# Kernel tuning notes

Measured on AMD Instinct MI355X. Metric: run time of the kernel, lower is better.

## Reference

```python
import jax, jax.numpy as jnp
import numpy as np

B, S, D, H, T = 64, 512, 1024, 1024, 9


def setup_inputs() -> dict:
    key = jax.random.key(0)
    ks = jax.random.split(key, 8)
    return {
        "input_": jax.random.normal(ks[0], (B, S, D), dtype=jnp.float32),
        "labels": jax.random.randint(ks[1], (B, S), 0, T),
        "attention_mask": jnp.ones((B, S), dtype=jnp.int32),
        # linear_1: input_dim -> hidden_dim (stored [in, out])
        "W1": (jax.random.normal(ks[2], (D, H), dtype=jnp.float32) * 0.02),
        "b1": jnp.zeros((H,), dtype=jnp.float32),
        # linear_2: hidden_dim -> tag_dim
        "W2": (jax.random.normal(ks[3], (H, T), dtype=jnp.float32) * 0.02),
        "b2": jnp.zeros((T,), dtype=jnp.float32),
        # torchcrf params: uniform(-0.1, 0.1)
        "start_trans": jax.random.uniform(ks[4], (T,), minval=-0.1, maxval=0.1),
        "end_trans": jax.random.uniform(ks[5], (T,), minval=-0.1, maxval=0.1),
        "trans": jax.random.uniform(ks[6], (T, T), minval=-0.1, maxval=0.1),
    }


def _crf_mean_llh(logits, tags, mask, start, end, trans):
    """torchcrf.CRF log-likelihood, reduction='mean'. logits [B,S,T]."""
    nb = logits.shape[0]
    em = jnp.transpose(logits, (1, 0, 2))          # [S,B,T] time-major
    tg = tags.T                                    # [S,B]
    m = mask.T.astype(logits.dtype)                # [S,B]
    bidx = jnp.arange(nb)

    # --- numerator: score of the gold path ---
    score0 = start[tg[0]] + em[0, bidx, tg[0]]

    def num_step(carry, x):
        score, last = carry
        em_t, tag_t, m_t = x
        score = score + (trans[last, tag_t] + em_t[bidx, tag_t]) * m_t
        last = jnp.where(m_t > 0, tag_t, last)
        return (score, last), None

    (score, last), _ = jax.lax.scan(num_step, (score0, tg[0]), (em[1:], tg[1:], m[1:]))
    score = score + end[last]

    # --- denominator: log-partition via logsumexp forward recurrence ---
    alpha0 = start[None, :] + em[0]                # [B,T]

    def part_step(alpha, x):
        em_t, m_t = x
        # [B, prev T, next T] semiring (log-sum-exp) matrix product
        nxt = jax.nn.logsumexp(alpha[:, :, None] + trans[None, :, :] + em_t[:, None, :], axis=1)
        alpha = jnp.where(m_t[:, None] > 0, nxt, alpha)
        return alpha, None

    alpha, _ = jax.lax.scan(part_step, alpha0, (em[1:], m[1:]))
    log_z = jax.nn.logsumexp(alpha + end[None, :], axis=1)

    return jnp.mean(score - log_z)


def reference(input_, labels, attention_mask, W1, b1, W2, b2, start_trans, end_trans, trans):
    # dropout layers are identity in eval mode
    h = input_ @ W1 + b1                           # [B,S,H]
    logits = h @ W2 + b2                           # [B,S,T]
    llh = _crf_mean_llh(logits, labels, attention_mask, start_trans, end_trans, trans)
    loss = -llh                                    # forward returns (-1*crf_llh, logits)
    return (loss, logits)
```

## Files before the change

### kernel.cpp

```cpp
#include <hip/hip_runtime.h>

#define BD 64
#define SD 512
#define DD 1024
#define HD 1024
#define TD 9
#define NSEG 16
#define SEGL 32
#define NEGI -1e30f

__device__ __forceinline__ float lse9(const float v[9]) {
    float m0 = fmaxf(v[0], v[1]);
    float m1 = fmaxf(v[2], v[3]);
    float m2 = fmaxf(v[4], v[5]);
    float m3 = fmaxf(v[6], v[7]);
    float mx = fmaxf(fmaxf(m0, m1), fmaxf(fmaxf(m2, m3), v[8]));
    float s = __expf(v[0] - mx) + __expf(v[1] - mx) + __expf(v[2] - mx)
            + __expf(v[3] - mx) + __expf(v[4] - mx) + __expf(v[5] - mx)
            + __expf(v[6] - mx) + __expf(v[7] - mx) + __expf(v[8] - mx);
    return mx + __logf(s);
}

__global__ __launch_bounds__(256) void k_w12(const float* __restrict__ W1,
                                             const float* __restrict__ b1,
                                             const float* __restrict__ W2,
                                             const float* __restrict__ b2,
                                             float* __restrict__ W12t,
                                             float* __restrict__ b12,
                                             float* __restrict__ out) {
    __shared__ float wred[4][TD];
    const int tid = threadIdx.x;
    const int wave = tid >> 6, lane = tid & 63;
    const int d = blockIdx.x;

    if (d == 0 && tid == 0) out[0] = 0.f;

    const float* row = (d < DD) ? (W1 + (size_t)d * HD) : b1;
    float4 x = ((const float4*)row)[tid];

    float w[36];
    const float4* wp = (const float4*)(W2 + (size_t)tid * 36);
#pragma unroll
    for (int u = 0; u < 9; u++) ((float4*)w)[u] = wp[u];

    float acc[TD];
#pragma unroll
    for (int t = 0; t < TD; t++)
        acc[t] = x.x * w[t] + x.y * w[9 + t] + x.z * w[18 + t] + x.w * w[27 + t];

#pragma unroll
    for (int t = 0; t < TD; t++) {
        float v = acc[t];
#pragma unroll
        for (int m = 1; m < 64; m <<= 1) v += __shfl_xor(v, m);
        acc[t] = v;
    }
    if (lane == 0) {
#pragma unroll
        for (int t = 0; t < TD; t++) wred[wave][t] = acc[t];
    }
    __syncthreads();
    if (tid < TD) {
        float s = wred[0][tid] + wred[1][tid] + wred[2][tid] + wred[3][tid];
        if (d < DD) W12t[tid * DD + d] = s;
        else        b12[tid] = s + b2[tid];
    }
}

__global__ __launch_bounds__(256) void k_gemm_seg(const float* __restrict__ X,
                                                  const float* __restrict__ W12t,
                                                  const float* __restrict__ b12,
                                                  const int* __restrict__ maskp,
                                                  const float* __restrict__ transp,
                                                  float* __restrict__ logits,
                                                  float* __restrict__ segP) {
    __shared__ float smem[TD * DD];
    __shared__ float em[SEGL * TD];
    __shared__ int   mk[SEGL];
    __shared__ float tr[81];
    __shared__ float bb[TD];

    const int blk = blockIdx.x;
    const int b = blk >> 4, s = blk & 15;
    const int tid = threadIdx.x;
    const int wave = tid >> 6, lane = tid & 63;
    const int g = lane >> 4, l16 = lane & 15;
    const int grp = wave * 4 + g;
    const int t0 = s * SEGL;

    for (int i = tid; i < TD * DD / 4; i += 256)
        ((float4*)smem)[i] = ((const float4*)W12t)[i];
    if (tid < TD) bb[tid] = b12[tid];
    if (tid < 81) tr[tid] = transp[tid];
    if (tid < SEGL) {
        int t = t0 + 1 + tid;
        mk[tid] = (t < SD) ? maskp[b * SD + t] : 0;
    }
    __syncthreads();

    const int rowa = t0 + 1 + grp * 2;
    const int rowb_real = rowa + 1;
    const int rowb = (rowb_real < SD) ? rowb_real : (SD - 1);

    const float4* xr0 = (const float4*)(X + ((size_t)b * SD + rowa) * DD);
    const float4* xr1 = (const float4*)(X + ((size_t)b * SD + rowb) * DD);

    float acc0[TD], acc1[TD];
#pragma unroll
    for (int t = 0; t < TD; t++) { acc0[t] = 0.f; acc1[t] = 0.f; }

#pragma unroll 4
    for (int k = 0; k < 16; k++) {
        int d4 = l16 + k * 16;
        float4 x0 = xr0[d4];
        float4 x1 = xr1[d4];
#pragma unroll
        for (int t = 0; t < TD; t++) {
            const float4 w = *(const float4*)&smem[t * DD + d4 * 4];
            acc0[t] += x0.x * w.x + x0.y * w.y + x0.z * w.z + x0.w * w.w;
            acc1[t] += x1.x * w.x + x1.y * w.y + x1.z * w.z + x1.w * w.w;
        }
    }

#pragma unroll
    for (int t = 0; t < TD; t++) {
        float v0 = acc0[t], v1 = acc1[t];
        v0 += __shfl_xor(v0, 1); v1 += __shfl_xor(v1, 1);
        v0 += __shfl_xor(v0, 2); v1 += __shfl_xor(v1, 2);
        v0 += __shfl_xor(v0, 4); v1 += __shfl_xor(v1, 4);
        v0 += __shfl_xor(v0, 8); v1 += __shfl_xor(v1, 8);
        acc0[t] = v0; acc1[t] = v1;
    }

    if (l16 < TD) {
        float v0 = acc0[l16] + bb[l16];
        float v1 = acc1[l16] + bb[l16];
        float* o = logits + ((size_t)b * SD + rowa) * TD;
        o[l16] = v0;
        em[(grp * 2) * TD + l16] = v0;
        if (rowb_real < SD) {
            o[TD + l16] = v1;
            em[(grp * 2 + 1) * TD + l16] = v1;
        }
    }

    if (s == 0 && grp == 0) {
        const float4* xr = (const float4*)(X + (size_t)b * SD * DD);
        float accz[TD];
#pragma unroll
        for (int t = 0; t < TD; t++) accz[t] = 0.f;
#pragma unroll 4
        for (int k = 0; k < 16; k++) {
            int d4 = l16 + k * 16;
            float4 xz = xr[d4];
#pragma unroll
            for (int t = 0; t < TD; t++) {
                const float4 w = *(const float4*)&smem[t * DD + d4 * 4];
                accz[t] += xz.x * w.x + xz.y * w.y + xz.z * w.z + xz.w * w.w;
            }
        }
#pragma unroll
        for (int t = 0; t < TD; t++) {
            float v = accz[t];
            v += __shfl_xor(v, 1);
            v += __shfl_xor(v, 2);
            v += __shfl_xor(v, 4);
            v += __shfl_xor(v, 8);
            accz[t] = v;
        }
        if (l16 < TD) logits[(size_t)b * SD * TD + l16] = accz[l16] + bb[l16];
    }
    __syncthreads();

    float* bufA = smem;
    float* bufB = smem + 16 * 81;

    for (int e = tid; e < 16 * 81; e += 256) {
        int p = e / 81, r = e - p * 81;
        int i = r / 9, j = r - i * 9;
        int la = 2 * p, lb = 2 * p + 1;
        int mA = mk[la], mB = mk[lb];
        float o;
        if (mA && mB) {
            float v[9];
#pragma unroll
            for (int k = 0; k < 9; k++)
                v[k] = tr[i * 9 + k] + em[la * 9 + k] + tr[k * 9 + j];
            o = lse9(v) + em[lb * 9 + j];
        } else if (mA) {
            o = tr[r] + em[la * 9 + j];
        } else if (mB) {
            o = tr[r] + em[lb * 9 + j];
        } else {
            o = (i == j) ? 0.f : NEGI;
        }
        bufA[e] = o;
    }
    __syncthreads();

#define COMBINE(SRC, DST, NP)                                        \
    for (int e = tid; e < (NP) * 81; e += 256) {                     \
        int p = e / 81, r = e - p * 81;                              \
        int i = r / 9, j = r - i * 9;                                \
        const float* Am = (SRC) + (2 * p) * 81;                      \
        const float* Bm = Am + 81;                                   \
        float v[9];                                                  \
        _Pragma("unroll")                                            \
        for (int k = 0; k < 9; k++) v[k] = Am[i * 9 + k] + Bm[k * 9 + j]; \
        (DST)[e] = lse9(v);                                          \
    }                                                                \
    __syncthreads();

    COMBINE(bufA, bufB, 8)
    COMBINE(bufB, bufA, 4)
    COMBINE(bufA, bufB, 2)

    if (tid < 81) {
        int i = tid / 9, j = tid - (tid / 9) * 9;
        float v[9];
#pragma unroll
        for (int k = 0; k < 9; k++) v[k] = bufB[i * 9 + k] + bufB[81 + k * 9 + j];
        segP[(size_t)blk * 81 + tid] = lse9(v);
    }
}

__global__ __launch_bounds__(256) void k_crf_fin(const float* __restrict__ logits,
                                                 const int* __restrict__ labels,
                                                 const int* __restrict__ maskp,
                                                 const float* __restrict__ startp,
                                                 const float* __restrict__ endp,
                                                 const float* __restrict__ transp,
                                                 const float* __restrict__ segP,
                                                 float* __restrict__ out) {
    const int b = blockIdx.x;
    const int tid = threadIdx.x;

    __shared__ float S[16 * 81];
    __shared__ float A8[8 * 81];
    __shared__ float A4[4 * 81];
    __shared__ float A2[2 * 81];
    __shared__ float P[81];
    __shared__ float finv[81];
    __shared__ float red[256];
    __shared__ int   redi[256];

    for (int i = tid; i < 16 * 81; i += 256) S[i] = segP[(size_t)b * NSEG * 81 + i];
    __syncthreads();

    COMBINE(S, A8, 8)
    COMBINE(A8, A4, 4)
    COMBINE(A4, A2, 2)

    if (tid < 81) {
        int i = tid / 9, j = tid - (tid / 9) * 9;
        float v[9];
#pragma unroll
        for (int k = 0; k < 9; k++) v[k] = A2[i * 9 + k] + A2[81 + k * 9 + j];
        P[tid] = lse9(v);
    }
    __syncthreads();

    if (tid < 81) {
        int k = tid / 9, j = tid - (tid / 9) * 9;
        finv[tid] = startp[k] + logits[(size_t)b * SD * TD + k] + P[tid] + endp[j];
    }

    float part = 0.f;
    for (int t = 1 + tid; t < SD; t += 256) {
        if (maskp[b * SD + t]) {
            int tgp = labels[b * SD + t - 1];
            int tgc = labels[b * SD + t];
            part += transp[tgp * TD + tgc] + logits[((size_t)b * SD + t) * TD + tgc];
        }
    }
    int lastt = 0;
    for (int t = tid; t < SD; t += 256) {
        if (maskp[b * SD + t]) lastt = max(lastt, t);
    }
    red[tid] = part;
    redi[tid] = lastt;
    __syncthreads();

    if (tid < 64) {
        float p4 = red[tid] + red[tid + 64] + red[tid + 128] + red[tid + 192];
        int l4 = max(max(redi[tid], redi[tid + 64]), max(redi[tid + 128], redi[tid + 192]));
#pragma unroll
        for (int m = 1; m < 64; m <<= 1) {
            p4 += __shfl_xor(p4, m);
            l4 = max(l4, __shfl_xor(l4, m));
        }
        float v1 = finv[tid];
        float v2 = (tid + 64 < 81) ? finv[tid + 64] : NEGI;
        float mx = fmaxf(v1, v2);
#pragma unroll
        for (int m = 1; m < 64; m <<= 1) mx = fmaxf(mx, __shfl_xor(mx, m));
        float ssum = __expf(v1 - mx) + __expf(v2 - mx);
#pragma unroll
        for (int m = 1; m < 64; m <<= 1) ssum += __shfl_xor(ssum, m);
        float logz = mx + __logf(ssum);

        if (tid == 0) {
            int tg0 = labels[b * SD];
            int tgl = labels[b * SD + l4];
            float score = p4 + startp[tg0] + logits[(size_t)b * SD * TD + tg0] + endp[tgl];
            atomicAdd(out, -(score - logz) / (float)BD);
        }
    }
}

extern "C" void kernel_launch(void* const* d_in, const int* in_sizes, int n_in,
                              void* d_out, int out_size, void* d_ws, size_t ws_size,
                              hipStream_t stream) {
    const float* X      = (const float*)d_in[0];
    const int*   labels = (const int*)d_in[1];
    const int*   maskp  = (const int*)d_in[2];
    const float* W1     = (const float*)d_in[3];
    const float* b1     = (const float*)d_in[4];
    const float* W2     = (const float*)d_in[5];
    const float* b2     = (const float*)d_in[6];
    const float* startp = (const float*)d_in[7];
    const float* endp   = (const float*)d_in[8];
    const float* transp = (const float*)d_in[9];

    float* out = (float*)d_out;
    float* ws = (float*)d_ws;

    float* W12t = ws + 64;
    float* b12  = ws + 64 + DD * TD;
    float* segP = ws + 64 + DD * TD + 16;
    float* logits = out + 1;

    hipLaunchKernelGGL(k_w12, dim3(DD + 1), dim3(256), 0, stream,
                       W1, b1, W2, b2, W12t, b12, out);
    hipLaunchKernelGGL(k_gemm_seg, dim3(BD * NSEG), dim3(256), 0, stream,
                       X, W12t, b12, maskp, transp, logits, segP);
    hipLaunchKernelGGL(k_crf_fin, dim3(BD), dim3(256), 0, stream,
                       logits, labels, maskp, startp, endp, transp, segP, out);
}
```

Baseline: 62.07 us.

## Remap gemm_seg to one row per 8-lane group with register-prefetched X, move row-0 to finisher

The segment GEMM now assigns one row per 8-thread group instead of two rows per 16-lane group. It also issues batched float4 loads of X into three register buffers, so more loads are in flight before the FMA work. The row-0 logits computation, previously done serially by one group in segment-0 blocks, moves into the CRF finisher kernel. That kernel reads a new d-major copy of W12 written by k_w12. Launch bounds request 4 blocks per CU. The larger register footprint could spill or limit occupancy, and the extra W12d write adds a small amount of traffic.

```diff
diff --git a/kernel.cpp b/kernel.cpp
--- a/kernel.cpp
+++ b/kernel.cpp
@@ -26,6 +26,7 @@
                                              const float* __restrict__ W2,
                                              const float* __restrict__ b2,
                                              float* __restrict__ W12t,
+                                             float* __restrict__ W12d,
                                              float* __restrict__ b12,
                                              float* __restrict__ out) {
     __shared__ float wred[4][TD];
@@ -62,18 +63,22 @@
     __syncthreads();
     if (tid < TD) {
         float s = wred[0][tid] + wred[1][tid] + wred[2][tid] + wred[3][tid];
-        if (d < DD) W12t[tid * DD + d] = s;
-        else        b12[tid] = s + b2[tid];
-    }
-}
-
-__global__ __launch_bounds__(256) void k_gemm_seg(const float* __restrict__ X,
-                                                  const float* __restrict__ W12t,
-                                                  const float* __restrict__ b12,
-                                                  const int* __restrict__ maskp,
-                                                  const float* __restrict__ transp,
-                                                  float* __restrict__ logits,
-                                                  float* __restrict__ segP) {
+        if (d < DD) {
+            W12t[tid * DD + d] = s;
+            W12d[d * TD + tid] = s;
+        } else {
+            b12[tid] = s + b2[tid];
+        }
+    }
+}
+
+__global__ __launch_bounds__(256, 4) void k_gemm_seg(const float* __restrict__ X,
+                                                     const float* __restrict__ W12t,
+                                                     const float* __restrict__ b12,
+                                                     const int* __restrict__ maskp,
+                                                     const float* __restrict__ transp,
+                                                     float* __restrict__ logits,
+                                                     float* __restrict__ segP) {
     __shared__ float smem[TD * DD];
     __shared__ float em[SEGL * TD];
     __shared__ int   mk[SEGL];
@@ -83,9 +88,8 @@
     const int blk = blockIdx.x;
     const int b = blk >> 4, s = blk & 15;
     const int tid = threadIdx.x;
-    const int wave = tid >> 6, lane = tid & 63;
-    const int g = lane >> 4, l16 = lane & 15;
-    const int grp = wave * 4 + g;
+    const int l8 = tid & 7;
+    const int grp = tid >> 3;
     const int t0 = s * SEGL;
 
     for (int i = tid; i < TD * DD / 4; i += 256)
@@ -98,77 +102,59 @@
     }
     __syncthreads();
 
-    const int rowa = t0 + 1 + grp * 2;
-    const int rowb_real = rowa + 1;
-    const int rowb = (rowb_real < SD) ? rowb_real : (SD - 1);
-
-    const float4* xr0 = (const float4*)(X + ((size_t)b * SD + rowa) * DD);
-    const float4* xr1 = (const float4*)(X + ((size_t)b * SD + rowb) * DD);
-
-    float acc0[TD], acc1[TD];
-#pragma unroll
-    for (int t = 0; t < TD; t++) { acc0[t] = 0.f; acc1[t] = 0.f; }
-
-#pragma unroll 4
-    for (int k = 0; k < 16; k++) {
-        int d4 = l16 + k * 16;
-        float4 x0 = xr0[d4];
-        float4 x1 = xr1[d4];
-#pragma unroll
-        for (int t = 0; t < TD; t++) {
-            const float4 w = *(const float4*)&smem[t * DD + d4 * 4];
-            acc0[t] += x0.x * w.x + x0.y * w.y + x0.z * w.z + x0.w * w.w;
-            acc1[t] += x1.x * w.x + x1.y * w.y + x1.z * w.z + x1.w * w.w;
-        }
-    }
+    const int rowa = t0 + 1 + grp;
+    const int rowc = (rowa < SD) ? rowa : (SD - 1);
+    const float4* xr = (const float4*)(X + ((size_t)b * SD + rowc) * DD);
+
+    float acc[TD];
+#pragma unroll
+    for (int t = 0; t < TD; t++) acc[t] = 0.f;
+
+#define GCOMPUTE(BUF, BASE)                                             \
+    _Pragma("unroll")                                                   \
+    for (int k = 0; k < 8; k++) {                                       \
+        const int d4 = l8 + (BASE) + k * 8;                             \
+        const float4 xv = BUF[k];                                       \
+        _Pragma("unroll")                                               \
+        for (int t = 0; t < TD; t++) {                                  \
+            const float4 w = *(const float4*)&smem[t * DD + d4 * 4];    \
+            acc[t] += xv.x * w.x + xv.y * w.y + xv.z * w.z + xv.w * w.w;\
+        }                                                               \
+    }
+
+    float4 xa[8], xb[8], xc[8];
+#pragma unroll
+    for (int k = 0; k < 8; k++) xa[k] = xr[l8 + k * 8];
+#pragma unroll
+    for (int k = 0; k < 8; k++) xb[k] = xr[l8 + 64 + k * 8];
+#pragma unroll
+    for (int k = 0; k < 8; k++) xc[k] = xr[l8 + 128 + k * 8];
+    GCOMPUTE(xa, 0)
+#pragma unroll
+    for (int k = 0; k < 8; k++) xa[k] = xr[l8 + 192 + k * 8];
+    GCOMPUTE(xb, 64)
+    GCOMPUTE(xc, 128)
+    GCOMPUTE(xa, 192)
 
 #pragma unroll
     for (int t = 0; t < TD; t++) {
-        float v0 = acc0[t], v1 = acc1[t];
-        v0 += __shfl_xor(v0, 1); v1 += __shfl_xor(v1, 1);
-        v0 += __shfl_xor(v0, 2); v1 += __shfl_xor(v1, 2);
-        v0 += __shfl_xor(v0, 4); v1 += __shfl_xor(v1, 4);
-        v0 += __shfl_xor(v0, 8); v1 += __shfl_xor(v1, 8);
-        acc0[t] = v0; acc1[t] = v1;
-    }
-
-    if (l16 < TD) {
-        float v0 = acc0[l16] + bb[l16];
-        float v1 = acc1[l16] + bb[l16];
-        float* o = logits + ((size_t)b * SD + rowa) * TD;
-        o[l16] = v0;
-        em[(grp * 2) * TD + l16] = v0;
-        if (rowb_real < SD) {
-            o[TD + l16] = v1;
-            em[(grp * 2 + 1) * TD + l16] = v1;
-        }
-    }
-
-    if (s == 0 && grp == 0) {
-        const float4* xr = (const float4*)(X + (size_t)b * SD * DD);
-        float accz[TD];
-#pragma unroll
-        for (int t = 0; t < TD; t++) accz[t] = 0.f;
-#pragma unroll 4
-        for (int k = 0; k < 16; k++) {
-            int d4 = l16 + k * 16;
-            float4 xz = xr[d4];
-#pragma unroll
-            for (int t = 0; t < TD; t++) {
-                const float4 w = *(const float4*)&smem[t * DD + d4 * 4];
-                accz[t] += xz.x * w.x + xz.y * w.y + xz.z * w.z + xz.w * w.w;
-            }
-        }
-#pragma unroll
-        for (int t = 0; t < TD; t++) {
-            float v = accz[t];
-            v += __shfl_xor(v, 1);
-            v += __shfl_xor(v, 2);
-            v += __shfl_xor(v, 4);
-            v += __shfl_xor(v, 8);
-            accz[t] = v;
-        }
-        if (l16 < TD) logits[(size_t)b * SD * TD + l16] = accz[l16] + bb[l16];
+        float v = acc[t];
+        v += __shfl_xor(v, 1);
+        v += __shfl_xor(v, 2);
+        v += __shfl_xor(v, 4);
+        acc[t] = v;
+    }
+
+    {
+        float v0 = acc[l8] + bb[l8];
+        float v8 = acc[8] + bb[8];
+        em[grp * TD + l8] = v0;
+        if (l8 == 0) em[grp * TD + 8] = v8;
+        if (rowa < SD) {
+            float* o = logits + ((size_t)b * SD + rowa) * TD;
+            o[l8] = v0;
+            if (l8 == 0) o[8] = v8;
+        }
     }
     __syncthreads();
 
@@ -224,16 +210,21 @@
     }
 }
 
-__global__ __launch_bounds__(256) void k_crf_fin(const float* __restrict__ logits,
+__global__ __launch_bounds__(256) void k_crf_fin(const float* __restrict__ X,
+                                                 const float* __restrict__ W12d,
+                                                 const float* __restrict__ b12,
+                                                 const float* __restrict__ logits,
                                                  const int* __restrict__ labels,
                                                  const int* __restrict__ maskp,
                                                  const float* __restrict__ startp,
                                                  const float* __restrict__ endp,
                                                  const float* __restrict__ transp,
                                                  const float* __restrict__ segP,
+                                                 float* __restrict__ logits_out0,
                                                  float* __restrict__ out) {
     const int b = blockIdx.x;
     const int tid = threadIdx.x;
+    const int wave = tid >> 6, lane = tid & 63;
 
     __shared__ float S[16 * 81];
     __shared__ float A8[8 * 81];
@@ -243,9 +234,40 @@
     __shared__ float finv[81];
     __shared__ float red[256];
     __shared__ int   redi[256];
+    __shared__ float wred[4][TD];
+    __shared__ float row0[TD];
+
+    {
+        float4 x = ((const float4*)(X + (size_t)b * SD * DD))[tid];
+        float w[36];
+        const float4* wp = (const float4*)(W12d + (size_t)tid * 36);
+#pragma unroll
+        for (int u = 0; u < 9; u++) ((float4*)w)[u] = wp[u];
+        float acc[TD];
+#pragma unroll
+        for (int t = 0; t < TD; t++)
+            acc[t] = x.x * w[t] + x.y * w[9 + t] + x.z * w[18 + t] + x.w * w[27 + t];
+#pragma unroll
+        for (int t = 0; t < TD; t++) {
+            float v = acc[t];
+#pragma unroll
+            for (int m = 1; m < 64; m <<= 1) v += __shfl_xor(v, m);
+            acc[t] = v;
+        }
+        if (lane == 0) {
+#pragma unroll
+            for (int t = 0; t < TD; t++) wred[wave][t] = acc[t];
+        }
+    }
 
     for (int i = tid; i < 16 * 81; i += 256) S[i] = segP[(size_t)b * NSEG * 81 + i];
     __syncthreads();
+
+    if (tid < TD) {
+        float v = wred[0][tid] + wred[1][tid] + wred[2][tid] + wred[3][tid] + b12[tid];
+        row0[tid] = v;
+        logits_out0[(size_t)b * SD * TD + tid] = v;
+    }
 
     COMBINE(S, A8, 8)
     COMBINE(A8, A4, 4)
@@ -262,7 +284,7 @@
 
     if (tid < 81) {
         int k = tid / 9, j = tid - (tid / 9) * 9;
-        finv[tid] = startp[k] + logits[(size_t)b * SD * TD + k] + P[tid] + endp[j];
+        finv[tid] = startp[k] + row0[k] + P[tid] + endp[j];
     }
 
     float part = 0.f;
@@ -302,7 +324,7 @@
         if (tid == 0) {
             int tg0 = labels[b * SD];
             int tgl = labels[b * SD + l4];
-            float score = p4 + startp[tg0] + logits[(size_t)b * SD * TD + tg0] + endp[tgl];
+            float score = p4 + startp[tg0] + row0[tg0] + endp[tgl];
             atomicAdd(out, -(score - logz) / (float)BD);
         }
     }
@@ -328,12 +350,14 @@
     float* W12t = ws + 64;
     float* b12  = ws + 64 + DD * TD;
     float* segP = ws + 64 + DD * TD + 16;
+    float* W12d = segP + (size_t)BD * NSEG * 81;
     float* logits = out + 1;
 
     hipLaunchKernelGGL(k_w12, dim3(DD + 1), dim3(256), 0, stream,
-                       W1, b1, W2, b2, W12t, b12, out);
+                       W1, b1, W2, b2, W12t, W12d, b12, out);
     hipLaunchKernelGGL(k_gemm_seg, dim3(BD * NSEG), dim3(256), 0, stream,
                        X, W12t, b12, maskp, transp, logits, segP);
     hipLaunchKernelGGL(k_crf_fin, dim3(BD), dim3(256), 0, stream,
-                       logits, labels, maskp, startp, endp, transp, segP, out);
-}
+                       X, W12d, b12, logits, labels, maskp, startp, endp, transp,
+                       segP, logits, out);
+}
```

Result: slower. 155.1 us (+149.9%).
